# Kernel tuning notes

Measured on AMD Instinct MI355X. Metric: run time of the kernel, lower is better.

## Reference

```python
import jax, jax.numpy as jnp
import numpy as np

B, S, C = 4, 2048, 1024
DK = C // 4   # 256, q/k projection dim
DO = 1024     # out_channels


def setup_inputs() -> dict:
    key = jax.random.key(0)
    ks = jax.random.split(key, 7)
    s = 1.0 / np.sqrt(C)
    return {
        "x": jax.random.normal(ks[0], (B, S, C), dtype=jnp.float32),
        "Wq": jax.random.uniform(ks[1], (C, DK), jnp.float32, -s, s),
        "bq": jax.random.uniform(ks[2], (DK,), jnp.float32, -s, s),
        "Wk": jax.random.uniform(ks[3], (C, DK), jnp.float32, -s, s),
        "bk": jax.random.uniform(ks[4], (DK,), jnp.float32, -s, s),
        "Wv": jax.random.uniform(ks[5], (C, DO), jnp.float32, -s, s),
        "bv": jax.random.uniform(ks[6], (DO,), jnp.float32, -s, s),
    }


def reference(x, Wq, bq, Wk, bk, Wv, bv):
    q = jnp.einsum("bsc,cd->bsd", x, Wq) + bq   # [B,S,DK]
    k = jnp.einsum("bsc,cd->bsd", x, Wk) + bk   # [B,S,DK]
    v = jnp.einsum("bsc,cd->bsd", x, Wv) + bv   # [B,S,DO]
    scores = jnp.einsum("bqd,bkd->bqk", q, k) / jnp.sqrt(jnp.float32(DK))
    attn = jax.nn.softmax(scores, axis=-1)      # [B,S,S]
    return jnp.einsum("bqk,bkd->bqd", attn, v)  # [B,S,DO]
```

## Files before the change

### kernel.cpp

```cpp
#include <hip/hip_runtime.h>
#include <hip/hip_bf16.h>

typedef __attribute__((ext_vector_type(8))) short short8;
typedef __attribute__((ext_vector_type(8))) __bf16 bf16x8;
typedef __attribute__((ext_vector_type(4))) float f32x4;

#define MFMA(a, b, c) __builtin_amdgcn_mfma_f32_16x16x32_bf16((a), (b), (c), 0, 0, 0)
#define SCALE 0.0625f

static __device__ __forceinline__ void gload16(const void* g, void* l) {
  __builtin_amdgcn_global_load_lds(
      (const __attribute__((address_space(1))) void*)g,
      (__attribute__((address_space(3))) void*)l, 16, 0, 0);
}

static __device__ __forceinline__ unsigned short f2b(float f) {
  union { __hip_bfloat16 h; unsigned short u; } cv;
  cv.h = __float2bfloat16(f);
  return cv.u;
}

__global__ __launch_bounds__(256) void prep_kern(
    const float* __restrict__ x, unsigned short* __restrict__ xb,
    const float* __restrict__ bq, const float* __restrict__ bk,
    const float* __restrict__ bv, float* __restrict__ bc,
    const float* __restrict__ Wq, const float* __restrict__ Wk,
    const float* __restrict__ Wv, unsigned short* __restrict__ wt) {
  __shared__ __align__(16) unsigned short tile[64][72];
  int bid = blockIdx.x, t = threadIdx.x;
  if (bid < 4096) {
    long i = ((long)bid * 256 + t) * 8;
    float4 a = *reinterpret_cast<const float4*>(x + i);
    float4 b = *reinterpret_cast<const float4*>(x + i + 4);
    short8 o;
    o[0] = (short)f2b(a.x); o[1] = (short)f2b(a.y); o[2] = (short)f2b(a.z); o[3] = (short)f2b(a.w);
    o[4] = (short)f2b(b.x); o[5] = (short)f2b(b.y); o[6] = (short)f2b(b.z); o[7] = (short)f2b(b.w);
    *reinterpret_cast<short8*>(xb + i) = o;
    return;
  }
  if (bid < 4102) {
    int i = (bid - 4096) * 256 + t;
    float v = (i < 256) ? bq[i] : (i < 512) ? bk[i - 256] : bv[i - 512];
    bc[i] = v;
    return;
  }
  const float* src; unsigned short* dst; int ldsrc, lam;
  if (bid < 4166)      { lam = bid - 4102; src = Wq; dst = wt;              ldsrc = 256;
                         lam = (lam & 3) | ((lam >> 2) << 8); }
  else if (bid < 4230) { lam = bid - 4166; src = Wk; dst = wt + 256 * 1024; ldsrc = 256;
                         lam = (lam & 3) | ((lam >> 2) << 8); }
  else                 { lam = bid - 4230; src = Wv; dst = wt + 512 * 1024; ldsrc = 1024;
                         lam = (lam & 15) | ((lam >> 4) << 8); }
  int c0 = (lam & 255) * 64, r0 = (lam >> 8) * 64;
  #pragma unroll
  for (int it = 0; it < 4; ++it) {
    int idx = it * 1024 + t * 4;
    int row = idx >> 6, col = idx & 63;
    float4 v = *reinterpret_cast<const float4*>(src + (long)(r0 + row) * ldsrc + c0 + col);
    tile[row][col + 0] = f2b(v.x); tile[row][col + 1] = f2b(v.y);
    tile[row][col + 2] = f2b(v.z); tile[row][col + 3] = f2b(v.w);
  }
  __syncthreads();
  #pragma unroll
  for (int it = 0; it < 4; ++it) {
    int idx = it * 1024 + t * 4;
    int orow = idx >> 6, ocol = idx & 63;
    ushort4 o;
    o.x = tile[ocol + 0][orow]; o.y = tile[ocol + 1][orow];
    o.z = tile[ocol + 2][orow]; o.w = tile[ocol + 3][orow];
    *reinterpret_cast<ushort4*>(dst + (long)(c0 + orow) * 1024 + r0 + ocol) = o;
  }
}

template <int SWZ, int BN, bool BIAS, bool VSPLIT, bool EXPSUM>
__global__ __launch_bounds__(512, 2) void gemm_pi(
    const unsigned short* __restrict__ A, const unsigned short* __restrict__ B,
    const float* __restrict__ bias, void* __restrict__ Cout,
    int NT, int lda, int ldb, int ldc,
    long batchA, long batchB, long batchC,
    float* __restrict__ lpart,
    unsigned short* __restrict__ vT) {
  constexpr int WM = 128;
  constexpr int WN = BN / 4;
  constexpr int NF = BN / 64;
  constexpr int BR = BN / 64;
  constexpr int ASH = 256 * 64;
  constexpr int TSH = ASH + BN * 64;
  __shared__ __align__(128) unsigned short lds[2 * TSH];

  int bid = blockIdx.x;
  int b = 0, tm, tn;
  if constexpr (SWZ == 0) {
    int xcd = bid & 7, s = bid >> 3;
    tm = xcd * 4 + (s >> 3); tn = s & 7;
  } else {
    int xcd = bid & 7, s = bid >> 3;
    b = xcd >> 1; tm = (xcd & 1) * 4 + (s >> 3); tn = s & 7;
  }

  int t = threadIdx.x, w = t >> 6, l = t & 63;
  int wr = w >> 2, wc = w & 3;
  int g = l >> 4, c = l & 15;

  f32x4 acc[8][NF];
  #pragma unroll
  for (int m = 0; m < 8; ++m)
    #pragma unroll
    for (int n = 0; n < NF; ++n) acc[m][n] = (f32x4){0.f, 0.f, 0.f, 0.f};

  int srow = t >> 3;
  int scb = (t & 7) * 16;
  const unsigned short* aptr = A + (long)b * batchA + (long)(tm * 256) * lda;
  const unsigned short* bptr = B + (long)b * batchB + (long)(tn * BN) * ldb;
  int kb = scb ^ ((srow & 7) << 4);

  auto stageA = [&](int buf, int k0, int r) {
    int row = r * 64 + srow;
    gload16(aptr + (long)row * lda + k0 + (kb >> 1),
            lds + buf * TSH + r * 4096 + t * 8);
  };
  auto stageB = [&](int buf, int k0, int r) {
    int row = r * 64 + srow;
    gload16(bptr + (long)row * ldb + k0 + (kb >> 1),
            lds + buf * TSH + ASH + r * 4096 + t * 8);
  };
  auto ldA = [&](const char* abase, int mh, int kh, int m) {
    int row = wr * WM + mh * 64 + m * 16 + c;
    int pb = row * 128 + (kh * 32 + g * 8) * 2;
    pb ^= ((pb >> 7) & 7) << 4;
    return *reinterpret_cast<const bf16x8*>(abase + pb);
  };
  auto ldB = [&](const char* bbase, int kh, int n) {
    int row = wc * WN + n * 16 + c;
    int pb = row * 128 + (kh * 32 + g * 8) * 2;
    pb ^= ((pb >> 7) & 7) << 4;
    return *reinterpret_cast<const bf16x8*>(bbase + pb);
  };

  #pragma unroll
  for (int r = 0; r < BR; ++r) stageB(0, 0, r);
  stageA(0, 0, 0); stageA(0, 0, 2); stageA(0, 0, 1); stageA(0, 0, 3);
  asm volatile("s_waitcnt vmcnt(0)" ::: "memory");
  __builtin_amdgcn_s_barrier();

  for (int kt = 0; kt < NT; ++kt) {
    int cur = kt & 1, nb = cur ^ 1;
    const char* abase = (const char*)(lds + cur * TSH);
    const char* bbase = (const char*)(lds + cur * TSH + ASH);
    bool more = (kt + 1) < NT;
    int k1 = (kt + 1) * 64;
    bf16x8 bfr[NF];
    #pragma unroll
    for (int p = 0; p < 4; ++p) {
      const int kh = p >> 1, mh = p & 1;
      bf16x8 af[4];
      #pragma unroll
      for (int m = 0; m < 4; ++m) af[m] = ldA(abase, mh, kh, m);
      if (mh == 0) {
        #pragma unroll
        for (int n = 0; n < NF; ++n) bfr[n] = ldB(bbase, kh, n);
      }
      if (more) {
        if constexpr (BN == 256) {
          if      (p == 0) { stageB(nb, k1, 0); stageB(nb, k1, 1); }
          else if (p == 1) { stageB(nb, k1, 2); stageB(nb, k1, 3); }
          else if (p == 2) { stageA(nb, k1, 0); stageA(nb, k1, 2); }
          else             { stageA(nb, k1, 1); stageA(nb, k1, 3); }
        } else {
          if      (p == 0) { stageB(nb, k1, 0); stageB(nb, k1, 1); stageB(nb, k1, 2); }
          else if (p == 1) { stageA(nb, k1, 0); stageA(nb, k1, 2); }
          else if (p == 2) { stageA(nb, k1, 1); stageA(nb, k1, 3); }
        }
      }
      __builtin_amdgcn_s_barrier();
      asm volatile("s_waitcnt lgkmcnt(0)" ::: "memory");
      __builtin_amdgcn_sched_barrier(0);
      __builtin_amdgcn_s_setprio(1);
      #pragma unroll
      for (int m = 0; m < 4; ++m)
        #pragma unroll
        for (int n = 0; n < NF; ++n)
          acc[mh * 4 + m][n] = MFMA(af[m], bfr[n], acc[mh * 4 + m][n]);
      __builtin_amdgcn_s_setprio(0);
      if (p == 0) {
        if (kt == NT - 1) asm volatile("s_waitcnt vmcnt(0)" ::: "memory");
        else if (BN == 256) asm volatile("s_waitcnt vmcnt(2)" ::: "memory");
        else                asm volatile("s_waitcnt vmcnt(3)" ::: "memory");
      }
      if (p == 3 && more) {
        asm volatile("s_waitcnt vmcnt(2)" ::: "memory");
      }
      __builtin_amdgcn_s_barrier();
    }
  }

  int rbase = tm * 256 + wr * WM + g * 4;
  int c0 = tn * BN + wc * WN + c;

  if constexpr (EXPSUM) {
    __shared__ float lred[4][256];
    #pragma unroll
    for (int mi = 0; mi < 8; ++mi) {
      int roff = (mi / 4) * 64 + (mi % 4) * 16;
      #pragma unroll
      for (int j = 0; j < 4; ++j) {
        long ob = (long)b * batchC + (long)(rbase + roff + j) * ldc + c0;
        float rs = 0.f;
        #pragma unroll
        for (int n = 0; n < NF; ++n) {
          float pv = __expf(acc[mi][n][j] * SCALE);
          ((unsigned short*)Cout)[ob + n * 16] = f2b(pv);
          rs += pv;
        }
        rs += __shfl_xor(rs, 1); rs += __shfl_xor(rs, 2);
        rs += __shfl_xor(rs, 4); rs += __shfl_xor(rs, 8);
        if (c == 0) lred[wc][wr * WM + roff + g * 4 + j] = rs;
      }
    }
    __syncthreads();
    for (int rr = t; rr < 256; rr += 512) {
      float s = lred[0][rr] + lred[1][rr] + lred[2][rr] + lred[3][rr];
      lpart[((long)b * 2048 + tm * 256 + rr) * 8 + tn] = s;
    }
  } else {
    #pragma unroll
    for (int mi = 0; mi < 8; ++mi) {
      int roff = (mi / 4) * 64 + (mi % 4) * 16;
      int s0 = (rbase + roff) & 2047;
      #pragma unroll
      for (int n = 0; n < NF; ++n) {
        int col = c0 + n * 16;
        float bv = BIAS ? bias[col] : 0.f;
        if (VSPLIT && (col - c) >= 512) {
          int bb = tm >> 3;
          ushort4 pk;
          pk.x = f2b(acc[mi][n][0] + bv); pk.y = f2b(acc[mi][n][1] + bv);
          pk.z = f2b(acc[mi][n][2] + bv); pk.w = f2b(acc[mi][n][3] + bv);
          *reinterpret_cast<ushort4*>(vT + (long)bb * 2097152 +
                                      (long)(col - 512) * 2048 + s0) = pk;
        } else {
          long rowb = (long)b * batchC + (long)(rbase + roff) * ldc + col;
          #pragma unroll
          for (int j = 0; j < 4; ++j)
            ((unsigned short*)Cout)[rowb + (long)j * ldc] = f2b(acc[mi][n][j] + bv);
        }
      }
    }
  }
}

__global__ __launch_bounds__(1024, 4) void gemm_pv(
    const unsigned short* __restrict__ A,
    const unsigned short* __restrict__ B,
    float* __restrict__ Cout,
    const float* __restrict__ linv) {
  constexpr int NT = 32;
  constexpr int ASH = 128 * 64;
  constexpr int TSH = ASH + 256 * 64;
  __shared__ __align__(128) unsigned short lds[3 * TSH];

  int bid = blockIdx.x;
  int xcd = bid & 7, sidx = bid >> 3;
  int b = xcd >> 1;
  int tm = (xcd & 1) * 8 + (sidx >> 2), tn = sidx & 3;

  int t = threadIdx.x, w = t >> 6, l = t & 63;
  int wr = w >> 2, wc = w & 3;
  int g = l >> 4, c = l & 15;

  f32x4 acc[2][4];
  #pragma unroll
  for (int m = 0; m < 2; ++m)
    #pragma unroll
    for (int n = 0; n < 4; ++n) acc[m][n] = (f32x4){0.f, 0.f, 0.f, 0.f};

  int srow = t >> 3;
  int scb = (t & 7) * 16;
  int kb = scb ^ ((srow & 7) << 4);
  const unsigned short* aptr = A + (long)b * 4194304 + (long)(tm * 128) * 2048;
  const unsigned short* bptr = B + (long)b * 2097152 + (long)(tn * 256) * 2048;

  auto stage3 = [&](int buf, int kt2) {
    int k0 = kt2 * 64;
    gload16(aptr + (long)srow * 2048 + k0 + (kb >> 1),
            lds + buf * TSH + t * 8);
    #pragma unroll
    for (int r = 0; r < 2; ++r) {
      int row = r * 128 + srow;
      gload16(bptr + (long)row * 2048 + k0 + (kb >> 1),
              lds + buf * TSH + ASH + r * 8192 + t * 8);
    }
  };

  stage3(0, 0); stage3(1, 1);
  asm volatile("s_waitcnt vmcnt(3)" ::: "memory");
  __builtin_amdgcn_s_barrier();

  for (int kt = 0; kt < NT; ++kt) {
    const char* abase = (const char*)(lds + (kt % 3) * TSH);
    const char* bbase = abase + ASH * 2;

    bf16x8 af[2][2], bf[2][4];
    #pragma unroll
    for (int sk = 0; sk < 2; ++sk) {
      #pragma unroll
      for (int m = 0; m < 2; ++m) {
        int p = (wr * 32 + m * 16 + c) * 128 + (sk * 32 + g * 8) * 2;
        p ^= ((p >> 7) & 7) << 4;
        af[sk][m] = *reinterpret_cast<const bf16x8*>(abase + p);
      }
      #pragma unroll
      for (int n = 0; n < 4; ++n) {
        int p = (wc * 64 + n * 16 + c) * 128 + (sk * 32 + g * 8) * 2;
        p ^= ((p >> 7) & 7) << 4;
        bf[sk][n] = *reinterpret_cast<const bf16x8*>(bbase + p);
      }
    }

    if (kt + 2 < NT) stage3((kt + 2) % 3, kt + 2);

    __builtin_amdgcn_s_setprio(1);
    #pragma unroll
    for (int sk = 0; sk < 2; ++sk)
      #pragma unroll
      for (int m = 0; m < 2; ++m)
        #pragma unroll
        for (int n = 0; n < 4; ++n)
          acc[m][n] = MFMA(af[sk][m], bf[sk][n], acc[m][n]);
    __builtin_amdgcn_s_setprio(0);

    if (kt < NT - 1) {
      if (kt == NT - 2) asm volatile("s_waitcnt vmcnt(0)" ::: "memory");
      else              asm volatile("s_waitcnt vmcnt(3)" ::: "memory");
      __builtin_amdgcn_s_barrier();
    }
  }

  int rbase = tm * 128 + wr * 32 + g * 4;
  int c0 = tn * 256 + wc * 64 + c;
  #pragma unroll
  for (int mi = 0; mi < 2; ++mi) {
    float lv[4];
    #pragma unroll
    for (int j = 0; j < 4; ++j)
      lv[j] = linv[(long)b * 2048 + rbase + mi * 16 + j];
    #pragma unroll
    for (int n = 0; n < 4; ++n) {
      long rowb = (long)b * 2097152 + (long)(rbase + mi * 16) * 1024 + c0 + n * 16;
      #pragma unroll
      for (int j = 0; j < 4; ++j)
        Cout[rowb + (long)j * 1024] = acc[mi][n][j] * lv[j];
    }
  }
}

__global__ __launch_bounds__(256) void linv_kern(const float* __restrict__ lpart,
                                                 float* __restrict__ linv) {
  int r = blockIdx.x * 256 + threadIdx.x;
  float s = 0.f;
  #pragma unroll
  for (int i = 0; i < 8; ++i) s += lpart[(long)r * 8 + i];
  linv[r] = 1.f / s;
}

extern "C" void kernel_launch(void* const* d_in, const int* in_sizes, int n_in,
                              void* d_out, int out_size, void* d_ws, size_t ws_size,
                              hipStream_t stream) {
  (void)in_sizes; (void)n_in; (void)out_size; (void)ws_size;
  const float* x  = (const float*)d_in[0];
  const float* Wq = (const float*)d_in[1];
  const float* bq = (const float*)d_in[2];
  const float* Wk = (const float*)d_in[3];
  const float* bk = (const float*)d_in[4];
  const float* Wv = (const float*)d_in[5];
  const float* bv = (const float*)d_in[6];
  float* out = (float*)d_out;
  char* ws = (char*)d_ws;

  unsigned short* xb   = (unsigned short*)(ws + 0);
  float*          lpart= (float*)         (ws + 0);
  float*          linv = (float*)         (ws + 262144);
  unsigned short* wt   = (unsigned short*)(ws + 16777216);
  float*          bc   = (float*)         (ws + 19922944);
  unsigned short* qkv  = (unsigned short*)(ws + 19929088);
  unsigned short* vT   = (unsigned short*)(ws + 45094912);
  unsigned short* attn = (unsigned short*)(ws + 61872128);

  prep_kern<<<4486, 256, 0, stream>>>(x, xb, bq, bk, bv, bc, Wq, Wk, Wv, wt);

  gemm_pi<0, 192, true, true, false><<<dim3(256), 512, 0, stream>>>(
      xb, wt, bc, qkv, 16, 1024, 1024, 1536, 0, 0, 0, nullptr, vT);

  gemm_pi<1, 256, false, false, true><<<dim3(256), 512, 0, stream>>>(
      qkv, qkv + 256, nullptr, attn, 4, 1536, 1536, 2048,
      (long)2048 * 1536, (long)2048 * 1536, (long)2048 * 2048, lpart, nullptr);
  linv_kern<<<32, 256, 0, stream>>>(lpart, linv);

  gemm_pv<<<dim3(256), 1024, 0, stream>>>(attn, vT, out, linv);
}
```

Measured before the change: 101.5 us.

## Load PV A-operand directly to registers and fold linv reduction into PV kernel

New measurement: 146.4 us. 44.2% more time.

```diff
diff --git a/kernel.cpp b/kernel.cpp
--- a/kernel.cpp
+++ b/kernel.cpp
@@ -253,11 +253,11 @@
     const unsigned short* __restrict__ A,
     const unsigned short* __restrict__ B,
     float* __restrict__ Cout,
-    const float* __restrict__ linv) {
+    const float* __restrict__ lpart) {
   constexpr int NT = 32;
-  constexpr int ASH = 128 * 64;
-  constexpr int TSH = ASH + 256 * 64;
-  __shared__ __align__(128) unsigned short lds[3 * TSH];
+  constexpr int BSH = 256 * 64;
+  __shared__ __align__(128) unsigned short lds[3 * BSH];
+  __shared__ float linv_s[128];
 
   int bid = blockIdx.x;
   int xcd = bid & 7, sidx = bid >> 3;
@@ -267,6 +267,12 @@
   int t = threadIdx.x, w = t >> 6, l = t & 63;
   int wr = w >> 2, wc = w & 3;
   int g = l >> 4, c = l & 15;
+
+  if (t < 128) {
+    const float* lp = lpart + ((long)b * 2048 + tm * 128 + t) * 8;
+    float s = lp[0] + lp[1] + lp[2] + lp[3] + lp[4] + lp[5] + lp[6] + lp[7];
+    linv_s[t] = 1.f / s;
+  }
 
   f32x4 acc[2][4];
   #pragma unroll
@@ -280,87 +286,87 @@
   const unsigned short* aptr = A + (long)b * 4194304 + (long)(tm * 128) * 2048;
   const unsigned short* bptr = B + (long)b * 2097152 + (long)(tn * 256) * 2048;
 
-  auto stage3 = [&](int buf, int kt2) {
+  auto stageB = [&](int buf, int kt2) {
     int k0 = kt2 * 64;
-    gload16(aptr + (long)srow * 2048 + k0 + (kb >> 1),
-            lds + buf * TSH + t * 8);
     #pragma unroll
     for (int r = 0; r < 2; ++r) {
       int row = r * 128 + srow;
       gload16(bptr + (long)row * 2048 + k0 + (kb >> 1),
-              lds + buf * TSH + ASH + r * 8192 + t * 8);
-    }
-  };
-
-  stage3(0, 0); stage3(1, 1);
-  asm volatile("s_waitcnt vmcnt(3)" ::: "memory");
+              lds + buf * BSH + r * 8192 + t * 8);
+    }
+  };
+
+  const unsigned short* arow0 = aptr + (long)(wr * 32 + c) * 2048;
+  const unsigned short* arow1 = aptr + (long)(wr * 32 + 16 + c) * 2048;
+  auto LOADA = [&](bf16x8 (&af)[2][2], int kt2) {
+    int k0 = kt2 * 64 + g * 8;
+    af[0][0] = *reinterpret_cast<const bf16x8*>(arow0 + k0);
+    af[0][1] = *reinterpret_cast<const bf16x8*>(arow1 + k0);
+    af[1][0] = *reinterpret_cast<const bf16x8*>(arow0 + k0 + 32);
+    af[1][1] = *reinterpret_cast<const bf16x8*>(arow1 + k0 + 32);
+  };
+
+  bf16x8 afA[2][2], afB[2][2];
+  LOADA(afA, 0);
+  stageB(0, 0); stageB(1, 1);
+  asm volatile("s_waitcnt vmcnt(2)" ::: "memory");
   __builtin_amdgcn_s_barrier();
 
-  for (int kt = 0; kt < NT; ++kt) {
-    const char* abase = (const char*)(lds + (kt % 3) * TSH);
-    const char* bbase = abase + ASH * 2;
-
-    bf16x8 af[2][2], bf[2][4];
-    #pragma unroll
-    for (int sk = 0; sk < 2; ++sk) {
-      #pragma unroll
-      for (int m = 0; m < 2; ++m) {
-        int p = (wr * 32 + m * 16 + c) * 128 + (sk * 32 + g * 8) * 2;
-        p ^= ((p >> 7) & 7) << 4;
-        af[sk][m] = *reinterpret_cast<const bf16x8*>(abase + p);
-      }
-      #pragma unroll
-      for (int n = 0; n < 4; ++n) {
-        int p = (wc * 64 + n * 16 + c) * 128 + (sk * 32 + g * 8) * 2;
-        p ^= ((p >> 7) & 7) << 4;
-        bf[sk][n] = *reinterpret_cast<const bf16x8*>(bbase + p);
-      }
-    }
-
-    if (kt + 2 < NT) stage3((kt + 2) % 3, kt + 2);
-
-    __builtin_amdgcn_s_setprio(1);
-    #pragma unroll
-    for (int sk = 0; sk < 2; ++sk)
-      #pragma unroll
-      for (int m = 0; m < 2; ++m)
-        #pragma unroll
-        for (int n = 0; n < 4; ++n)
-          acc[m][n] = MFMA(af[sk][m], bf[sk][n], acc[m][n]);
-    __builtin_amdgcn_s_setprio(0);
-
-    if (kt < NT - 1) {
-      if (kt == NT - 2) asm volatile("s_waitcnt vmcnt(0)" ::: "memory");
-      else              asm volatile("s_waitcnt vmcnt(3)" ::: "memory");
-      __builtin_amdgcn_s_barrier();
-    }
-  }
-
-  int rbase = tm * 128 + wr * 32 + g * 4;
+#define PV_TILE(T, CUR, NXT)                                                 \
+  {                                                                          \
+    const char* bb = (const char*)(lds + ((T) % 3) * BSH);                   \
+    if ((T) + 1 < NT) LOADA(NXT, (T) + 1);                                   \
+    if ((T) + 2 < NT) stageB(((T) + 2) % 3, (T) + 2);                        \
+    bf16x8 bf[2][4];                                                         \
+    _Pragma("unroll")                                                        \
+    for (int sk = 0; sk < 2; ++sk) {                                         \
+      _Pragma("unroll")                                                      \
+      for (int n = 0; n < 4; ++n) {                                          \
+        int p = (wc * 64 + n * 16 + c) * 128 + (sk * 32 + g * 8) * 2;        \
+        p ^= ((p >> 7) & 7) << 4;                                            \
+        bf[sk][n] = *reinterpret_cast<const bf16x8*>(bb + p);                 \
+      }                                                                      \
+    }                                                                        \
+    __builtin_amdgcn_s_setprio(1);                                           \
+    _Pragma("unroll")                                                        \
+    for (int sk = 0; sk < 2; ++sk) {                                         \
+      _Pragma("unroll")                                                      \
+      for (int m = 0; m < 2; ++m) {                                          \
+        _Pragma("unroll")                                                    \
+        for (int n = 0; n < 4; ++n)                                          \
+          acc[m][n] = MFMA(CUR[sk][m], bf[sk][n], acc[m][n]);                \
+      }                                                                      \
+    }                                                                        \
+    __builtin_amdgcn_s_setprio(0);                                           \
+    if ((T) < NT - 1) {                                                      \
+      asm volatile("s_waitcnt vmcnt(2)" ::: "memory");                       \
+      __builtin_amdgcn_s_barrier();                                          \
+    }                                                                        \
+  }
+
+  for (int kt = 0; kt < NT; kt += 2) {
+    PV_TILE(kt, afA, afB)
+    PV_TILE(kt + 1, afB, afA)
+  }
+#undef PV_TILE
+
+  int rloc = wr * 32 + g * 4;
   int c0 = tn * 256 + wc * 64 + c;
   #pragma unroll
   for (int mi = 0; mi < 2; ++mi) {
     float lv[4];
     #pragma unroll
     for (int j = 0; j < 4; ++j)
-      lv[j] = linv[(long)b * 2048 + rbase + mi * 16 + j];
+      lv[j] = linv_s[rloc + mi * 16 + j];
     #pragma unroll
     for (int n = 0; n < 4; ++n) {
-      long rowb = (long)b * 2097152 + (long)(rbase + mi * 16) * 1024 + c0 + n * 16;
+      long rowb = (long)b * 2097152 + (long)(tm * 128 + rloc + mi * 16) * 1024
+                + c0 + n * 16;
       #pragma unroll
       for (int j = 0; j < 4; ++j)
         Cout[rowb + (long)j * 1024] = acc[mi][n][j] * lv[j];
     }
   }
-}
-
-__global__ __launch_bounds__(256) void linv_kern(const float* __restrict__ lpart,
-                                                 float* __restrict__ linv) {
-  int r = blockIdx.x * 256 + threadIdx.x;
-  float s = 0.f;
-  #pragma unroll
-  for (int i = 0; i < 8; ++i) s += lpart[(long)r * 8 + i];
-  linv[r] = 1.f / s;
 }
 
 extern "C" void kernel_launch(void* const* d_in, const int* in_sizes, int n_in,
@@ -379,7 +385,6 @@
 
   unsigned short* xb   = (unsigned short*)(ws + 0);
   float*          lpart= (float*)         (ws + 0);
-  float*          linv = (float*)         (ws + 262144);
   unsigned short* wt   = (unsigned short*)(ws + 16777216);
   float*          bc   = (float*)         (ws + 19922944);
   unsigned short* qkv  = (unsigned short*)(ws + 19929088);
@@ -394,7 +399,6 @@
   gemm_pi<1, 256, false, false, true><<<dim3(256), 512, 0, stream>>>(
       qkv, qkv + 256, nullptr, attn, 4, 1536, 1536, 2048,
       (long)2048 * 1536, (long)2048 * 1536, (long)2048 * 2048, lpart, nullptr);
-  linv_kern<<<32, 256, 0, stream>>>(lpart, linv);
-
-  gemm_pv<<<dim3(256), 1024, 0, stream>>>(attn, vT, out, linv);
-}
+
+  gemm_pv<<<dim3(256), 1024, 0, stream>>>(attn, vT, out, lpart);
+}
```
